# Optimization experiments

Measured on AMD Instinct MI355X. Metric: run time of the kernel, lower is better.

## Reference

```python
import jax, jax.numpy as jnp
import numpy as np

B, S, D = 2, 2048, 1024          # batch, seq, n_embd
E, GS, K = 8, 4, 2               # num_experts, group_size, top-k
H = 2 * D                        # hidden_dim of SharedExpertMLP
A = H // 16                      # adapt_dim = 128
G = E // GS                      # num_groups
LN_EPS = 1e-5


def _ln(z, g, b):
    mu = jnp.mean(z, -1, keepdims=True)
    v = jnp.mean((z - mu) ** 2, -1, keepdims=True)
    return (z - mu) * jax.lax.rsqrt(v + LN_EPS) * g + b


def setup_inputs() -> dict:
    key = jax.random.key(0)
    ks = jax.random.split(key, 12)
    s = float(D) ** -0.5
    sa = s * 0.01
    se = 0.01 * float(A) ** -0.5
    n = lambda k, shape, std: jax.random.normal(k, shape, jnp.float32) * std
    return {
        'x': jax.random.normal(ks[0], (B, S, D), jnp.float32),
        'W_up': n(ks[1], (H, D), s),
        'W_gate': n(ks[2], (H, D), s),
        'W_down': n(ks[3], (D, H), s),
        'W_pre': n(ks[4], (A, D), sa),
        'W_post': n(ks[5], (A, H), sa),
        'ln_g': jnp.ones((A,), jnp.float32),
        'ln_b': jnp.zeros((A,), jnp.float32),
        'W_aproj': n(ks[6], (H, A), sa),
        'A_exp': n(ks[7], (E, A, A), se),
        'ln_g_e': jnp.ones((E, A), jnp.float32),
        'ln_b_e': jnp.zeros((E, A), jnp.float32),
        'W_eproj': n(ks[8], (H, A), se),
        'W_oproj': n(ks[9], (D, H), se),
        'W_rg': n(ks[10], (G, D), 0.001),
        'W_re': n(ks[11], (GS, D), 0.001),
    }


def reference(x, W_up, W_gate, W_down, W_pre, W_post, ln_g, ln_b, W_aproj,
              A_exp, ln_g_e, ln_b_e, W_eproj, W_oproj, W_rg, W_re):
    silu = jax.nn.silu
    # ---- SharedExpertMLP ----
    up = x @ W_up.T
    gate = x @ W_gate.T
    hidden = silu(gate) * up                               # [B,S,H]
    adapt_in = _ln(x @ W_pre.T, ln_g, ln_b)                # [B,S,A]
    adapt_out = _ln(hidden @ W_post.T, ln_g, ln_b)         # [B,S,A]
    aw = silu(jnp.clip(jnp.einsum('bsa,bta->bst', adapt_in, adapt_out), -5.0, 5.0))
    adapt = jnp.einsum('bst,bta->bsa', aw, adapt_in)
    hidden = hidden + 0.1 * (adapt @ W_aproj.T)
    shared = hidden @ W_down.T                             # [B,S,D]
    # ---- HierarchicalRouter ----
    gl = x @ W_rg.T                                        # [B,S,G]
    gp = jax.nn.softmax(gl, -1)
    gw = jnp.max(gp, -1)                                   # top-1 group weight
    gidx = jnp.argmax(gp, -1)
    el = x @ W_re.T                                        # [B,S,GS]
    ep = jax.nn.softmax(el, -1)
    wloc, iloc = jax.lax.top_k(ep, K)
    eidx = gidx[..., None] * GS + iloc                     # [B,S,K] global expert ids
    wloc = wloc / (jnp.sum(wloc, -1, keepdims=True) + 1e-7)
    fw = gw[..., None] * wloc                              # final weights
    N = B * S
    dm = jnp.zeros((N, E), x.dtype).at[
        jnp.arange(N)[:, None], eidx.reshape(N, K)].set(fw.reshape(N, K))
    load = dm.sum(0)
    target = load.sum() / E
    router_loss = 0.001 * (jnp.mean((load - target) ** 2)
                           + jnp.mean(gl ** 2) + jnp.mean(el ** 2))
    dm = dm.reshape(B, S, E)
    # ---- ExpertGroup combine (vectorized masked gather/MLP/scatter) ----
    pre = x @ W_pre.T                                      # [B,S,A]
    h_e = jnp.einsum('bsa,eca->ebsc', pre, A_exp)          # per-expert adapter
    h_e = _ln(h_e, ln_g_e[:, None, None, :], ln_b_e[:, None, None, :])
    contrib = jnp.einsum('ebsc,hc->ebsh', h_e, W_eproj)    # [E,B,S,H]
    contrib = jnp.einsum('ebsh,dh->ebsd', contrib, W_oproj)
    w_e = jnp.moveaxis(dm, -1, 0)                          # [E,B,S]
    out = jnp.sum(dm, -1)[..., None] * shared + 0.1 * jnp.einsum('ebsd,ebs->bsd', contrib, w_e)
    return out, router_loss
```

## Files before the change

kernel.cpp:

```cpp
#include <hip/hip_runtime.h>
#include <hip/hip_bf16.h>
#include <math.h>

static constexpr int Bc = 2;
static constexpr int Sc = 2048;
static constexpr int Dc = 1024;
static constexpr int Hc = 2048;
static constexpr int Ac = 128;
static constexpr int Ec = 8;
static constexpr int GSc = 4;
static constexpr int Gc = 2;
static constexpr int Nc = Bc * Sc;
static constexpr float LN_EPSc = 1e-5f;
static constexpr int RBLK = 512;

typedef __attribute__((ext_vector_type(8))) short bf16x8;
typedef __attribute__((ext_vector_type(4))) float f32x4;
typedef __attribute__((ext_vector_type(4))) unsigned short us4;

__device__ __forceinline__ unsigned short f2b(float f) {
    union { float f; unsigned u; } v; v.f = f;
    return (unsigned short)((v.u + 0x7FFFu + ((v.u >> 16) & 1u)) >> 16);
}
__device__ __forceinline__ float b2f(unsigned short h) {
    union { unsigned u; float f; } v; v.u = (unsigned)h << 16; return v.f;
}
__device__ __forceinline__ float fsilu(float x) {
    return x / (1.f + __expf(-x));
}

#define GLOAD16(g, l) __builtin_amdgcn_global_load_lds( \
    (const __attribute__((address_space(1))) void*)(g), \
    (__attribute__((address_space(3))) void*)(l), 16, 0, 0)

template<int EPI>
__global__ __launch_bounds__(256, 4) void mgemm(
    const unsigned short* __restrict__ Ag, const unsigned short* __restrict__ Bg,
    void* __restrict__ Cg, int N, int K, int lda, int ldb, float alpha,
    float* __restrict__ aux, void* __restrict__ aux2,
    long long sA, long long sB, long long sC)
{
    __shared__ unsigned short As[128 * 32];
    __shared__ unsigned short Bs[128 * 32];
    const unsigned short* A = Ag + (long long)blockIdx.z * sA;
    const unsigned short* B = Bg + (long long)blockIdx.z * sB;
    float* fC = (float*)Cg + (long long)blockIdx.z * sC;
    unsigned short* usC = (unsigned short*)Cg + (long long)blockIdx.z * sC;

    const int nwg = gridDim.x * gridDim.y;
    const int flat = blockIdx.y * gridDim.x + blockIdx.x;
    const int swz = (flat & 7) * (nwg >> 3) + (flat >> 3);
    const int bx = swz % gridDim.x, by = swz / gridDim.x;
    const int bm = by * 128, bn = bx * 128;

    const int tid = threadIdx.x;
    const int w = tid >> 6, l = tid & 63;
    const int wm = (w >> 1) * 64, wn = (w & 1) * 64;
    const int fr = l & 15, g = l >> 4;

    const f32x4 zero = { 0.f, 0.f, 0.f, 0.f };
    f32x4 acc[4][4];
    #pragma unroll
    for (int i = 0; i < 4; ++i)
        #pragma unroll
        for (int j = 0; j < 4; ++j) acc[i][j] = zero;

    for (int k0 = 0; k0 < K; k0 += 32) {
        #pragma unroll
        for (int p = 0; p < 2; ++p) {
            const int c = p * 256 + tid;
            GLOAD16(A + (long long)(bm + (c >> 2)) * lda + k0 + (c & 3) * 8, &As[c * 8]);
            GLOAD16(B + (long long)(bn + (c >> 2)) * ldb + k0 + (c & 3) * 8, &Bs[c * 8]);
        }
        __syncthreads();
        bf16x8 af[4], bfv[4];
        #pragma unroll
        for (int i = 0; i < 4; ++i) {
            af[i]  = *(const bf16x8*)&As[(wm + i * 16 + fr) * 32 + g * 8];
            bfv[i] = *(const bf16x8*)&Bs[(wn + i * 16 + fr) * 32 + g * 8];
        }
        #pragma unroll
        for (int i = 0; i < 4; ++i)
            #pragma unroll
            for (int j = 0; j < 4; ++j)
                acc[i][j] = __builtin_amdgcn_mfma_f32_16x16x32_bf16(af[i], bfv[j], acc[i][j], 0, 0, 0);
        __syncthreads();
    }

    if (EPI == 9) {
        if (bn < 2 * Hc) {
            #pragma unroll
            for (int mi = 0; mi < 4; ++mi) {
                #pragma unroll
                for (int j = 0; j < 2; ++j) {
                    #pragma unroll
                    for (int jr = 0; jr < 4; ++jr) {
                        const long long row = bm + wm + mi * 16 + g * 4 + jr;
                        const long long colh = ((bn + wn) >> 1) + j * 16 + fr;
                        const float gv = acc[mi][2 * j][jr];
                        const float uv = acc[mi][2 * j + 1][jr];
                        usC[row * Hc + colh] = f2b(fsilu(gv) * uv);
                    }
                }
            }
        } else {
            unsigned short* preb = (unsigned short*)aux2;
            #pragma unroll
            for (int mi = 0; mi < 4; ++mi) {
                #pragma unroll
                for (int ni = 0; ni < 4; ++ni) {
                    #pragma unroll
                    for (int jr = 0; jr < 4; ++jr) {
                        const long long row = bm + wm + mi * 16 + g * 4 + jr;
                        const int lc = wn + ni * 16 + fr;
                        const float v = acc[mi][ni][jr];
                        aux[row * Ac + lc] = v;
                        preb[row * Ac + lc] = f2b(v);
                    }
                }
            }
        }
    } else {
        #pragma unroll
        for (int mi = 0; mi < 4; ++mi)
            #pragma unroll
            for (int ni = 0; ni < 4; ++ni)
                #pragma unroll
                for (int jr = 0; jr < 4; ++jr) {
                    const long long row = bm + wm + mi * 16 + g * 4 + jr;
                    const long long col = bn + wn + ni * 16 + fr;
                    const long long idx = row * (long long)N + col;
                    const float v = acc[mi][ni][jr];
                    if (EPI == 0) fC[idx] = v;
                    else usC[idx] = f2b(alpha * v);
                }
    }
}

__global__ __launch_bounds__(256, 2) void mgemm64(
    const unsigned short* __restrict__ Ag, const unsigned short* __restrict__ Bg,
    float* __restrict__ Cg, int N, int K, int lda, int ldb, int zmod,
    long long sA1, long long sB1, long long sC1,
    long long sA2, long long sB2, long long sC2)
{
    __shared__ unsigned short As[128 * 32];
    __shared__ unsigned short Bs[64 * 32];
    const int z1 = blockIdx.z % zmod, z2 = blockIdx.z / zmod;
    const unsigned short* A = Ag + (long long)z1 * sA1 + (long long)z2 * sA2;
    const unsigned short* B = Bg + (long long)z1 * sB1 + (long long)z2 * sB2;
    float* fC = Cg + (long long)z1 * sC1 + (long long)z2 * sC2;

    const int nwg = gridDim.x * gridDim.y;
    const int flat = blockIdx.y * gridDim.x + blockIdx.x;
    const int swz = (flat & 7) * (nwg >> 3) + (flat >> 3);
    const int bx = swz % gridDim.x, by = swz / gridDim.x;
    const int bm = by * 128, bn = bx * 64;

    const int tid = threadIdx.x;
    const int w = tid >> 6, l = tid & 63;
    const int wm = (w >> 1) * 64, wn = (w & 1) * 32;
    const int fr = l & 15, g = l >> 4;

    const f32x4 zero = { 0.f, 0.f, 0.f, 0.f };
    f32x4 acc[4][2];
    #pragma unroll
    for (int i = 0; i < 4; ++i)
        #pragma unroll
        for (int j = 0; j < 2; ++j) acc[i][j] = zero;

    for (int k0 = 0; k0 < K; k0 += 32) {
        #pragma unroll
        for (int p = 0; p < 2; ++p) {
            const int c = p * 256 + tid;
            GLOAD16(A + (long long)(bm + (c >> 2)) * lda + k0 + (c & 3) * 8, &As[c * 8]);
        }
        GLOAD16(B + (long long)(bn + (tid >> 2)) * ldb + k0 + (tid & 3) * 8, &Bs[tid * 8]);
        __syncthreads();
        bf16x8 af[4], bfv[2];
        #pragma unroll
        for (int i = 0; i < 4; ++i)
            af[i]  = *(const bf16x8*)&As[(wm + i * 16 + fr) * 32 + g * 8];
        #pragma unroll
        for (int j = 0; j < 2; ++j)
            bfv[j] = *(const bf16x8*)&Bs[(wn + j * 16 + fr) * 32 + g * 8];
        #pragma unroll
        for (int i = 0; i < 4; ++i)
            #pragma unroll
            for (int j = 0; j < 2; ++j)
                acc[i][j] = __builtin_amdgcn_mfma_f32_16x16x32_bf16(af[i], bfv[j], acc[i][j], 0, 0, 0);
        __syncthreads();
    }

    #pragma unroll
    for (int mi = 0; mi < 4; ++mi)
        #pragma unroll
        for (int ni = 0; ni < 2; ++ni)
            #pragma unroll
            for (int jr = 0; jr < 4; ++jr) {
                const long long row = bm + wm + mi * 16 + g * 4 + jr;
                const long long col = bn + wn + ni * 16 + fr;
                fC[row * (long long)N + col] = acc[mi][ni][jr];
            }
}

__global__ __launch_bounds__(256, 2) void fadapt_k(
    const unsigned short* __restrict__ adapt_in,
    const unsigned short* __restrict__ adapt_out,
    const unsigned short* __restrict__ adapt_inT,
    float* __restrict__ partial)
{
    __shared__ unsigned short P_lds[4 * 128 * 32];
    __shared__ unsigned short Bs[128 * 32];

    const int b = blockIdx.z;
    const int q0 = blockIdx.y * 128;
    const int t0 = blockIdx.x * 256;

    const unsigned short* Qg = adapt_in + (long long)b * Sc * Ac;
    const unsigned short* Kg = adapt_out + (long long)b * Sc * Ac;
    const unsigned short* Vt = adapt_inT + (long long)b * Ac * Sc;

    const int tid = threadIdx.x;
    const int w = tid >> 6, l = tid & 63;
    const int wm = (w >> 1) * 64, wn = (w & 1) * 64;
    const int fr = l & 15, g = l >> 4;

    bf16x8 qf[4][4];
    for (int ks = 0; ks < 4; ++ks) {
        #pragma unroll
        for (int p = 0; p < 2; ++p) {
            const int c = p * 256 + tid;
            GLOAD16(Qg + (long long)(q0 + (c >> 2)) * Ac + ks * 32 + (c & 3) * 8, &Bs[c * 8]);
        }
        __syncthreads();
        #pragma unroll
        for (int i = 0; i < 4; ++i)
            qf[i][ks] = *(const bf16x8*)&Bs[(wm + i * 16 + fr) * 32 + g * 8];
        __syncthreads();
    }

    const f32x4 zero = { 0.f, 0.f, 0.f, 0.f };
    f32x4 acc[4][4];
    #pragma unroll
    for (int i = 0; i < 4; ++i)
        #pragma unroll
        for (int j = 0; j < 4; ++j) acc[i][j] = zero;

    #pragma unroll 1
    for (int ts = 0; ts < 2; ++ts) {
        const int t1 = t0 + ts * 128;
        f32x4 sacc[4][4];
        #pragma unroll
        for (int i = 0; i < 4; ++i)
            #pragma unroll
            for (int j = 0; j < 4; ++j) sacc[i][j] = zero;
        for (int ks = 0; ks < 4; ++ks) {
            #pragma unroll
            for (int p = 0; p < 2; ++p) {
                const int c = p * 256 + tid;
                GLOAD16(Kg + (long long)(t1 + (c >> 2)) * Ac + ks * 32 + (c & 3) * 8, &Bs[c * 8]);
            }
            __syncthreads();
            bf16x8 bfv[4];
            #pragma unroll
            for (int j = 0; j < 4; ++j)
                bfv[j] = *(const bf16x8*)&Bs[(wn + j * 16 + fr) * 32 + g * 8];
            #pragma unroll
            for (int i = 0; i < 4; ++i)
                #pragma unroll
                for (int j = 0; j < 4; ++j)
                    sacc[i][j] = __builtin_amdgcn_mfma_f32_16x16x32_bf16(qf[i][ks], bfv[j], sacc[i][j], 0, 0, 0);
            __syncthreads();
        }
        #pragma unroll
        for (int mi = 0; mi < 4; ++mi) {
            #pragma unroll
            for (int ni = 0; ni < 4; ++ni) {
                const int t = wn + ni * 16 + fr;
                const int base = (t >> 5) * 4096 + (t & 31);
                #pragma unroll
                for (int jr = 0; jr < 4; ++jr) {
                    const int row = wm + mi * 16 + g * 4 + jr;
                    float v = sacc[mi][ni][jr];
                    v = fminf(fmaxf(v, -5.f), 5.f);
                    P_lds[base + row * 32] = f2b(fsilu(v));
                }
            }
        }
        __syncthreads();
        for (int ks = 0; ks < 4; ++ks) {
            #pragma unroll
            for (int p = 0; p < 2; ++p) {
                const int c = p * 256 + tid;
                GLOAD16(Vt + (long long)(c >> 2) * Sc + t1 + ks * 32 + (c & 3) * 8, &Bs[c * 8]);
            }
            __syncthreads();
            bf16x8 af[4], bfv[4];
            #pragma unroll
            for (int i = 0; i < 4; ++i)
                af[i] = *(const bf16x8*)&P_lds[ks * 4096 + (wm + i * 16 + fr) * 32 + g * 8];
            #pragma unroll
            for (int j = 0; j < 4; ++j)
                bfv[j] = *(const bf16x8*)&Bs[(wn + j * 16 + fr) * 32 + g * 8];
            #pragma unroll
            for (int i = 0; i < 4; ++i)
                #pragma unroll
                for (int j = 0; j < 4; ++j)
                    acc[i][j] = __builtin_amdgcn_mfma_f32_16x16x32_bf16(af[i], bfv[j], acc[i][j], 0, 0, 0);
            __syncthreads();
        }
    }

    float* op = partial + ((long long)blockIdx.x * Bc + b) * Sc * Ac;
    #pragma unroll
    for (int mi = 0; mi < 4; ++mi)
        #pragma unroll
        for (int ni = 0; ni < 4; ++ni)
            #pragma unroll
            for (int jr = 0; jr < 4; ++jr) {
                const long long row = q0 + wm + mi * 16 + g * 4 + jr;
                const long long col = wn + ni * 16 + fr;
                op[row * Ac + col] = acc[mi][ni][jr];
            }
}

__global__ __launch_bounds__(256, 2) void final_k(
    const unsigned short* __restrict__ hidden, const unsigned short* __restrict__ Wd,
    const unsigned short* __restrict__ adaptb, const unsigned short* __restrict__ Wdap,
    const unsigned short* __restrict__ h2v, const unsigned short* __restrict__ Wopep,
    const float* __restrict__ dmsum, float* __restrict__ out)
{
    __shared__ unsigned short As[128 * 32];
    __shared__ unsigned short Bs[64 * 32];

    const int nwg = gridDim.x * gridDim.y;
    const int flat = blockIdx.y * gridDim.x + blockIdx.x;
    const int swz = (flat & 7) * (nwg >> 3) + (flat >> 3);
    const int bx = swz % gridDim.x, by = swz / gridDim.x;
    const int bm = by * 128, bn = bx * 64;

    const int tid = threadIdx.x;
    const int w = tid >> 6, l = tid & 63;
    const int wm = (w >> 1) * 64, wn = (w & 1) * 32;
    const int fr = l & 15, g = l >> 4;

    const f32x4 zero = { 0.f, 0.f, 0.f, 0.f };
    f32x4 acc[4][2];
    #pragma unroll
    for (int i = 0; i < 4; ++i)
        #pragma unroll
        for (int j = 0; j < 2; ++j) acc[i][j] = zero;

    const unsigned short* Ap[3] = { hidden, adaptb, h2v };
    const unsigned short* Bp[3] = { Wd, Wdap, Wopep };
    const int Ks[3]  = { Hc, Ac, Ac };
    const int lds[3] = { Hc, Ac, Ac };

    #pragma unroll 1
    for (int ph = 0; ph < 3; ++ph) {
        if (ph == 2) {
            #pragma unroll
            for (int mi = 0; mi < 4; ++mi)
                #pragma unroll
                for (int jr = 0; jr < 4; ++jr) {
                    const float rs = dmsum[bm + wm + mi * 16 + g * 4 + jr];
                    #pragma unroll
                    for (int ni = 0; ni < 2; ++ni) acc[mi][ni][jr] *= rs;
                }
        }
        const unsigned short* A = Ap[ph];
        const unsigned short* B = Bp[ph];
        const int K = Ks[ph], ld = lds[ph];
        for (int k0 = 0; k0 < K; k0 += 32) {
            #pragma unroll
            for (int p = 0; p < 2; ++p) {
                const int c = p * 256 + tid;
                GLOAD16(A + (long long)(bm + (c >> 2)) * ld + k0 + (c & 3) * 8, &As[c * 8]);
            }
            GLOAD16(B + (long long)(bn + (tid >> 2)) * ld + k0 + (tid & 3) * 8, &Bs[tid * 8]);
            __syncthreads();
            bf16x8 af[4], bfv[2];
            #pragma unroll
            for (int i = 0; i < 4; ++i)
                af[i]  = *(const bf16x8*)&As[(wm + i * 16 + fr) * 32 + g * 8];
            #pragma unroll
            for (int j = 0; j < 2; ++j)
                bfv[j] = *(const bf16x8*)&Bs[(wn + j * 16 + fr) * 32 + g * 8];
            #pragma unroll
            for (int i = 0; i < 4; ++i)
                #pragma unroll
                for (int j = 0; j < 2; ++j)
                    acc[i][j] = __builtin_amdgcn_mfma_f32_16x16x32_bf16(af[i], bfv[j], acc[i][j], 0, 0, 0);
            __syncthreads();
        }
    }

    #pragma unroll
    for (int mi = 0; mi < 4; ++mi)
        #pragma unroll
        for (int ni = 0; ni < 2; ++ni)
            #pragma unroll
            for (int jr = 0; jr < 4; ++jr) {
                const long long row = bm + wm + mi * 16 + g * 4 + jr;
                const long long col = bn + wn + ni * 16 + fr;
                out[row * (long long)Dc + col] = acc[mi][ni][jr];
            }
}

template<int NP, int BF>
__global__ __launch_bounds__(256) void reduce_k(const float* __restrict__ in,
                                                void* __restrict__ outp,
                                                long long pstride, int n4, float alpha)
{
    for (int i = blockIdx.x * 256 + threadIdx.x; i < n4; i += gridDim.x * 256) {
        float4 s = ((const float4*)in)[i];
        #pragma unroll
        for (int p = 1; p < NP; ++p) {
            const float4 v = ((const float4*)(in + (long long)p * pstride))[i];
            s.x += v.x; s.y += v.y; s.z += v.z; s.w += v.w;
        }
        s.x *= alpha; s.y *= alpha; s.z *= alpha; s.w *= alpha;
        if (BF) {
            us4 o = { f2b(s.x), f2b(s.y), f2b(s.z), f2b(s.w) };
            ((us4*)outp)[i] = o;
        } else {
            ((float4*)outp)[i] = s;
        }
    }
}

struct CastJobs {
    const float* src[4];
    unsigned short* dst[4];
    int n4[4];
};
__global__ __launch_bounds__(256) void cast_k(CastJobs jobs) {
    const int b = blockIdx.y;
    const float4* s = (const float4*)jobs.src[b];
    us4* d = (us4*)jobs.dst[b];
    const int n = jobs.n4[b];
    for (int i = blockIdx.x * 256 + threadIdx.x; i < n; i += gridDim.x * 256) {
        const float4 v = s[i];
        us4 o;
        o.x = f2b(v.x); o.y = f2b(v.y); o.z = f2b(v.z); o.w = f2b(v.w);
        d[i] = o;
    }
}

__global__ __launch_bounds__(256) void gucast_k(const float* __restrict__ Wg,
                                                const float* __restrict__ Wu,
                                                const float* __restrict__ Wpre,
                                                unsigned short* __restrict__ Wcat)
{
    const int r = blockIdx.x;
    const float* src;
    int srcrow;
    if (r < 2 * Hc) {
        const int b = r >> 5, w = r & 31;
        src = (w < 16) ? Wg : Wu;
        srcrow = b * 16 + (w & 15);
    } else {
        src = Wpre;
        srcrow = r - 2 * Hc;
    }
    const float4 v = ((const float4*)(src + (long long)srcrow * Dc))[threadIdx.x];
    us4 o;
    o.x = f2b(v.x); o.y = f2b(v.y); o.z = f2b(v.z); o.w = f2b(v.w);
    ((us4*)(Wcat + (long long)r * Dc))[threadIdx.x] = o;
}

__global__ __launch_bounds__(256) void ct_k(const float* __restrict__ in0,
                                            const float* __restrict__ in1,
                                            unsigned short* __restrict__ out0,
                                            unsigned short* __restrict__ out1)
{
    const float* in = blockIdx.z ? in1 : in0;
    unsigned short* out = blockIdx.z ? out1 : out0;
    const int t0 = blockIdx.x * 64, a0 = blockIdx.y * 64;
    __shared__ float T[64][68];
    const int rr = threadIdx.x >> 4, cc = (threadIdx.x & 15) * 4;
    #pragma unroll
    for (int p = 0; p < 4; ++p) {
        const int row = p * 16 + rr;
        *(float4*)&T[row][cc] = *(const float4*)&in[(long long)(t0 + row) * Ac + a0 + cc];
    }
    __syncthreads();
    #pragma unroll
    for (int p = 0; p < 4; ++p) {
        const int ar = p * 16 + rr;
        us4 o;
        o.x = f2b(T[cc + 0][ar]); o.y = f2b(T[cc + 1][ar]);
        o.z = f2b(T[cc + 2][ar]); o.w = f2b(T[cc + 3][ar]);
        *(us4*)&out[(long long)(a0 + ar) * Hc + t0 + cc] = o;
    }
}

__global__ __launch_bounds__(64) void ln_k(const float* __restrict__ in, unsigned short* __restrict__ out,
                                           const float* __restrict__ gg, const float* __restrict__ bb)
{
    const int row = blockIdx.x;
    const int lane = threadIdx.x;
    const float z0 = in[(long long)row * 128 + lane];
    const float z1 = in[(long long)row * 128 + 64 + lane];
    float s = z0 + z1;
    for (int o = 32; o > 0; o >>= 1) s += __shfl_down(s, o, 64);
    s = __shfl(s, 0, 64);
    const float mu = s * (1.f / 128.f);
    const float d0 = z0 - mu, d1 = z1 - mu;
    float v = d0 * d0 + d1 * d1;
    for (int o = 32; o > 0; o >>= 1) v += __shfl_down(v, o, 64);
    v = __shfl(v, 0, 64);
    const float r = rsqrtf(v * (1.f / 128.f) + LN_EPSc);
    out[(long long)row * 128 + lane] = f2b(d0 * r * gg[lane] + bb[lane]);
    out[(long long)row * 128 + 64 + lane] = f2b(d1 * r * gg[lane + 64] + bb[lane + 64]);
}

__global__ __launch_bounds__(64) void redln_k(const float* __restrict__ in,
                                              unsigned short* __restrict__ out,
                                              const float* __restrict__ gg,
                                              const float* __restrict__ bb,
                                              long long pstride)
{
    const int row = blockIdx.x;
    const int lane = threadIdx.x;
    float z0 = 0.f, z1 = 0.f;
    #pragma unroll
    for (int p = 0; p < 4; ++p) {
        z0 += in[p * pstride + (long long)row * 128 + lane];
        z1 += in[p * pstride + (long long)row * 128 + 64 + lane];
    }
    float s = z0 + z1;
    for (int o = 32; o > 0; o >>= 1) s += __shfl_down(s, o, 64);
    s = __shfl(s, 0, 64);
    const float mu = s * (1.f / 128.f);
    const float d0 = z0 - mu, d1 = z1 - mu;
    float v = d0 * d0 + d1 * d1;
    for (int o = 32; o > 0; o >>= 1) v += __shfl_down(v, o, 64);
    v = __shfl(v, 0, 64);
    const float r = rsqrtf(v * (1.f / 128.f) + LN_EPSc);
    out[(long long)row * 128 + lane] = f2b(d0 * r * gg[lane] + bb[lane]);
    out[(long long)row * 128 + 64 + lane] = f2b(d1 * r * gg[lane + 64] + bb[lane + 64]);
}

__global__ __launch_bounds__(256) void trans_k(const unsigned short* __restrict__ in,
                                               unsigned short* __restrict__ out)
{
    const int z = blockIdx.z;
    const int t0 = blockIdx.x * 64, a0 = blockIdx.y * 64;
    __shared__ unsigned short T[64][72];
    const unsigned short* ip = in + (long long)z * Sc * Ac;
    unsigned short* op = out + (long long)z * Ac * Sc;
    const int rr = threadIdx.x >> 4, cc = (threadIdx.x & 15) * 4;
    #pragma unroll
    for (int p = 0; p < 4; ++p) {
        const int row = p * 16 + rr;
        *(us4*)&T[row][cc] = *(const us4*)&ip[(long long)(t0 + row) * Ac + a0 + cc];
    }
    __syncthreads();
    #pragma unroll
    for (int p = 0; p < 4; ++p) {
        const int arow = p * 16 + rr;
        us4 o;
        o.x = T[cc + 0][arow]; o.y = T[cc + 1][arow];
        o.z = T[cc + 2][arow]; o.w = T[cc + 3][arow];
        *(us4*)&op[(long long)(a0 + arow) * Sc + t0 + cc] = o;
    }
}

__global__ __launch_bounds__(256) void router_k(const float* __restrict__ x,
                                                const float* __restrict__ W_rg,
                                                const float* __restrict__ W_re,
                                                int* __restrict__ eidx, float* __restrict__ fw,
                                                float* __restrict__ dmsum,
                                                float* __restrict__ rpart,
                                                unsigned short* __restrict__ xb)
{
    const int wv = threadIdx.x >> 6;
    const int lane = threadIdx.x & 63;
    float load8[8] = {0.f, 0.f, 0.f, 0.f, 0.f, 0.f, 0.f, 0.f};
    float sqg = 0.f, sqe = 0.f;

    #pragma unroll
    for (int it = 0; it < 2; ++it) {
        const int t = blockIdx.x * 8 + wv * 2 + it;
        const float* xr = x + (long long)t * Dc;
        float a0 = 0, a1 = 0, a2 = 0, a3 = 0, a4 = 0, a5 = 0;
        #pragma unroll
        for (int j = 0; j < 16; ++j) {
            const int d = lane + 64 * j;
            const float xv = xr[d];
            xb[(long long)t * Dc + d] = f2b(xv);
            a0 += xv * W_rg[d];          a1 += xv * W_rg[Dc + d];
            a2 += xv * W_re[d];          a3 += xv * W_re[Dc + d];
            a4 += xv * W_re[2 * Dc + d]; a5 += xv * W_re[3 * Dc + d];
        }
        #pragma unroll
        for (int o = 32; o > 0; o >>= 1) {
            a0 += __shfl_xor(a0, o, 64); a1 += __shfl_xor(a1, o, 64);
            a2 += __shfl_xor(a2, o, 64); a3 += __shfl_xor(a3, o, 64);
            a4 += __shfl_xor(a4, o, 64); a5 += __shfl_xor(a5, o, 64);
        }
        if (lane == 0) {
            const float gl0 = a0, gl1 = a1;
            const float m = fmaxf(gl0, gl1);
            const float e0 = expf(gl0 - m), e1 = expf(gl1 - m);
            const float inv = 1.f / (e0 + e1);
            const float gp0 = e0 * inv, gp1 = e1 * inv;
            const int gidx = (gl1 > gl0) ? 1 : 0;
            const float gw = fmaxf(gp0, gp1);
            float el[4] = { a2, a3, a4, a5 };
            const float me = fmaxf(fmaxf(el[0], el[1]), fmaxf(el[2], el[3]));
            float ep[4]; float se = 0.f;
            #pragma unroll
            for (int i = 0; i < 4; ++i) { ep[i] = expf(el[i] - me); se += ep[i]; }
            const float invs = 1.f / se;
            #pragma unroll
            for (int i = 0; i < 4; ++i) ep[i] *= invs;
            int i0 = 0;
            #pragma unroll
            for (int i = 1; i < 4; ++i) if (ep[i] > ep[i0]) i0 = i;
            int i1 = -1;
            #pragma unroll
            for (int i = 0; i < 4; ++i) { if (i == i0) continue; if (i1 < 0 || ep[i] > ep[i1]) i1 = i; }
            const float w0 = ep[i0], w1 = ep[i1];
            const float sn = w0 + w1 + 1e-7f;
            const float f0 = gw * w0 / sn, f1 = gw * w1 / sn;
            const int ei0 = gidx * GSc + i0, ei1 = gidx * GSc + i1;
            eidx[t * 2] = ei0; eidx[t * 2 + 1] = ei1;
            fw[t * 2] = f0; fw[t * 2 + 1] = f1;
            dmsum[t] = f0 + f1;
            #pragma unroll
            for (int e = 0; e < 8; ++e)
                load8[e] += ((e == ei0) ? f0 : 0.f) + ((e == ei1) ? f1 : 0.f);
            sqg += gl0 * gl0 + gl1 * gl1;
            sqe += el[0] * el[0] + el[1] * el[1] + el[2] * el[2] + el[3] * el[3];
        }
    }
    __shared__ float sh[4][10];
    if (lane == 0) {
        #pragma unroll
        for (int e = 0; e < 8; ++e) sh[wv][e] = load8[e];
        sh[wv][8] = sqg; sh[wv][9] = sqe;
    }
    __syncthreads();
    if (threadIdx.x < 10) {
        rpart[blockIdx.x * 10 + threadIdx.x] =
            sh[0][threadIdx.x] + sh[1][threadIdx.x] + sh[2][threadIdx.x] + sh[3][threadIdx.x];
    }
}

__global__ __launch_bounds__(512) void loss_k(const float* __restrict__ rpart,
                                              float* __restrict__ out_loss)
{
    const int tid = threadIdx.x;
    const int lane = tid & 63, wv = tid >> 6;
    float v[10];
    #pragma unroll
    for (int c = 0; c < 10; ++c) v[c] = rpart[tid * 10 + c];
    #pragma unroll
    for (int o = 32; o > 0; o >>= 1)
        #pragma unroll
        for (int c = 0; c < 10; ++c) v[c] += __shfl_xor(v[c], o, 64);
    __shared__ float sh[8][10];
    if (lane == 0) {
        #pragma unroll
        for (int c = 0; c < 10; ++c) sh[wv][c] = v[c];
    }
    __syncthreads();
    if (tid == 0) {
        float load[8]; float sqg = 0.f, sqe = 0.f;
        #pragma unroll
        for (int e = 0; e < 8; ++e) load[e] = 0.f;
        for (int wvi = 0; wvi < 8; ++wvi) {
            #pragma unroll
            for (int e = 0; e < 8; ++e) load[e] += sh[wvi][e];
            sqg += sh[wvi][8]; sqe += sh[wvi][9];
        }
        float s = 0.f;
        for (int e = 0; e < Ec; ++e) s += load[e];
        const float tgt = s / (float)Ec;
        float var = 0.f;
        for (int e = 0; e < Ec; ++e) { const float d = load[e] - tgt; var += d * d; }
        var /= (float)Ec;
        const float l = var + sqg / (float)(Nc * Gc) + sqe / (float)(Nc * GSc);
        *out_loss = 0.001f * l;
    }
}

__global__ __launch_bounds__(128) void combine_k(const float* __restrict__ h_dense,
                                                 const float* __restrict__ ln_g_e,
                                                 const float* __restrict__ ln_b_e,
                                                 const int* __restrict__ eidx,
                                                 const float* __restrict__ fw,
                                                 unsigned short* __restrict__ h2)
{
    const int t = blockIdx.x;
    const int tid = threadIdx.x;
    __shared__ float red[2];

    float acc = 0.f;
    #pragma unroll
    for (int slot = 0; slot < 2; ++slot) {
        const int e = eidx[t * 2 + slot];
        const float w = fw[t * 2 + slot];
        const float h = h_dense[((long long)e * Nc + t) * 128 + tid];
        float v = h;
        for (int o = 32; o > 0; o >>= 1) v += __shfl_down(v, o, 64);
        if ((tid & 63) == 0) red[tid >> 6] = v;
        __syncthreads();
        const float mu = (red[0] + red[1]) * (1.f / 128.f);
        __syncthreads();
        const float d = h - mu;
        v = d * d;
        for (int o = 32; o > 0; o >>= 1) v += __shfl_down(v, o, 64);
        if ((tid & 63) == 0) red[tid >> 6] = v;
        __syncthreads();
        const float var = (red[0] + red[1]) * (1.f / 128.f);
        __syncthreads();
        acc += w * (d * rsqrtf(var + LN_EPSc) * ln_g_e[e * 128 + tid] + ln_b_e[e * 128 + tid]);
    }
    h2[(long long)t * 128 + tid] = f2b(acc);
}

extern "C" void kernel_launch(void* const* d_in, const int* in_sizes, int n_in,
                              void* d_out, int out_size, void* d_ws, size_t ws_size,
                              hipStream_t stream)
{
    const float* x       = (const float*)d_in[0];
    const float* W_up    = (const float*)d_in[1];
    const float* W_gate  = (const float*)d_in[2];
    const float* W_down  = (const float*)d_in[3];
    const float* W_pre   = (const float*)d_in[4];
    const float* W_post  = (const float*)d_in[5];
    const float* ln_g    = (const float*)d_in[6];
    const float* ln_b    = (const float*)d_in[7];
    const float* W_aproj = (const float*)d_in[8];
    const float* A_exp   = (const float*)d_in[9];
    const float* ln_g_e  = (const float*)d_in[10];
    const float* ln_b_e  = (const float*)d_in[11];
    const float* W_eproj = (const float*)d_in[12];
    const float* W_oproj = (const float*)d_in[13];
    const float* W_rg    = (const float*)d_in[14];
    const float* W_re    = (const float*)d_in[15];

    float* out = (float*)d_out;

    char* p = (char*)d_ws;
    auto alloc = [&](size_t bytes) { void* r = (void*)p; p += (bytes + 255) & ~(size_t)255; return r; };
    float* pre      = (float*)alloc((size_t)Nc * Ac * 4);
    float* h_dense  = (float*)alloc((size_t)Ec * Nc * Ac * 4);
    float* rpart    = (float*)alloc((size_t)RBLK * 10 * 4);
    float* fw       = (float*)alloc((size_t)Nc * 2 * 4);
    float* dmsum    = (float*)alloc((size_t)Nc * 4);
    int*   eidx     = (int*)alloc((size_t)Nc * 2 * 4);
    unsigned short* xb      = (unsigned short*)alloc((size_t)Nc * Dc * 2);
    unsigned short* Wcat_b  = (unsigned short*)alloc((size_t)(2 * Hc + Ac) * Dc * 2);
    unsigned short* Wd_b    = (unsigned short*)alloc((size_t)Dc * Hc * 2);
    unsigned short* Wop_b   = (unsigned short*)alloc((size_t)Dc * Hc * 2);
    unsigned short* Wpost_b = (unsigned short*)alloc((size_t)Ac * Hc * 2);
    unsigned short* WapT_b  = (unsigned short*)alloc((size_t)Ac * Hc * 2);
    unsigned short* WepT_b  = (unsigned short*)alloc((size_t)Ac * Hc * 2);
    unsigned short* Wdap_b  = (unsigned short*)alloc((size_t)Dc * Ac * 2);
    unsigned short* Wopep_b = (unsigned short*)alloc((size_t)Dc * Ac * 2);
    unsigned short* Aexp_b  = (unsigned short*)alloc((size_t)Ec * Ac * Ac * 2);
    unsigned short* pre_b   = (unsigned short*)alloc((size_t)Nc * Ac * 2);
    unsigned short* hidden  = (unsigned short*)alloc((size_t)Nc * Hc * 2);
    unsigned short* adapt_in  = (unsigned short*)alloc((size_t)Nc * Ac * 2);
    unsigned short* adapt_inT = (unsigned short*)alloc((size_t)Nc * Ac * 2);
    unsigned short* adapt_out = (unsigned short*)alloc((size_t)Nc * Ac * 2);
    unsigned short* adaptb    = (unsigned short*)alloc((size_t)Nc * Ac * 2);
    unsigned short* h2        = (unsigned short*)alloc((size_t)Nc * Ac * 2);

    float* wprepP = h_dense;
    float* postP  = h_dense;
    float* adaptP = h_dense;

    CastJobs jobs;
    jobs.src[0] = W_down;  jobs.dst[0] = Wd_b;    jobs.n4[0] = Dc * Hc / 4;
    jobs.src[1] = W_oproj; jobs.dst[1] = Wop_b;   jobs.n4[1] = Dc * Hc / 4;
    jobs.src[2] = W_post;  jobs.dst[2] = Wpost_b; jobs.n4[2] = Ac * Hc / 4;
    jobs.src[3] = A_exp;   jobs.dst[3] = Aexp_b;  jobs.n4[3] = Ec * Ac * Ac / 4;
    cast_k<<<dim3(128, 4), 256, 0, stream>>>(jobs);
    gucast_k<<<2 * Hc + Ac, 256, 0, stream>>>(W_gate, W_up, W_pre, Wcat_b);
    ct_k<<<dim3(Hc / 64, Ac / 64, 2), 256, 0, stream>>>(W_aproj, W_eproj, WapT_b, WepT_b);

    router_k<<<RBLK, 256, 0, stream>>>(x, W_rg, W_re, eidx, fw, dmsum, rpart, xb);
    loss_k<<<1, 512, 0, stream>>>(rpart, out + (size_t)Nc * Dc);

    mgemm64<<<dim3(2, 8, 8), 256, 0, stream>>>(Wd_b, WapT_b, wprepP, Ac, 512, Hc, Hc,
        2,
        (long long)Dc * Hc, (long long)Ac * Hc, (long long)Dc * Ac,
        512, 512, (long long)2 * Dc * Ac);
    reduce_k<4, 1><<<256, 256, 0, stream>>>(wprepP, Wdap_b,
        (long long)2 * Dc * Ac, 2 * Dc * Ac / 4, 0.1f);

    mgemm<9><<<dim3(33, 32), 256, 0, stream>>>(xb, Wcat_b, hidden, 2 * Hc + Ac, Dc, Dc, Dc, 0.f,
        pre, pre_b, 0, 0, 0);
    ln_k<<<Nc, 64, 0, stream>>>(pre, adapt_in, ln_g, ln_b);
    trans_k<<<dim3(Sc / 64, Ac / 64, Bc), 256, 0, stream>>>(adapt_in, adapt_inT);

    mgemm64<<<dim3(2, 32, 4), 256, 0, stream>>>(hidden, Wpost_b, postP, Ac, 512, Hc, Hc,
        8, 512, 512, (long long)Nc * Ac, 0, 0, 0);
    redln_k<<<Nc, 64, 0, stream>>>(postP, adapt_out, ln_g, ln_b, (long long)Nc * Ac);

    mgemm64<<<dim3(2, 32, Ec), 256, 0, stream>>>(pre_b, Aexp_b, h_dense, Ac, Ac, Ac, Ac,
        16, 0, (long long)Ac * Ac, (long long)Nc * Ac, 0, 0, 0);
    combine_k<<<Nc, 128, 0, stream>>>(h_dense, ln_g_e, ln_b_e, eidx, fw, h2);

    fadapt_k<<<dim3(8, 16, 2), 256, 0, stream>>>(adapt_in, adapt_out, adapt_inT, adaptP);
    reduce_k<8, 1><<<512, 256, 0, stream>>>(adaptP, adaptb,
        (long long)2 * Sc * Ac, 2 * Sc * Ac / 4, 1.f);

    final_k<<<dim3(Dc / 64, Nc / 128), 256, 0, stream>>>(
        hidden, Wd_b, adaptb, Wdap_b, h2, Wopep_b, dmsum, out);
}
```

Measured before the change: 200.7 us.

## Double GEMM K-tile with XOR-swizzled LDS, merge prep kernels, fuse LN with transpose

The main GEMM and the final GEMM now stage 64-wide K tiles instead of 32, halving the number of barrier pairs per K sweep, and use an XOR swizzle on the LDS chunk index to cut bank conflicts. The three weight cast/transpose kernels are merged into one launch. LayerNorm of the pre-adapter output is fused with its transpose into one kernel, and the warp reductions switch to xor-shuffles. Doubling LDS per block may lower occupancy on the mgemm kernel, which declares four blocks per CU.

```diff
diff --git a/kernel.cpp b/kernel.cpp
--- a/kernel.cpp
+++ b/kernel.cpp
@@ -40,8 +40,8 @@
     float* __restrict__ aux, void* __restrict__ aux2,
     long long sA, long long sB, long long sC)
 {
-    __shared__ unsigned short As[128 * 32];
-    __shared__ unsigned short Bs[128 * 32];
+    __shared__ unsigned short As[128 * 64];
+    __shared__ unsigned short Bs[128 * 64];
     const unsigned short* A = Ag + (long long)blockIdx.z * sA;
     const unsigned short* B = Bg + (long long)blockIdx.z * sB;
     float* fC = (float*)Cg + (long long)blockIdx.z * sC;
@@ -65,25 +65,32 @@
         #pragma unroll
         for (int j = 0; j < 4; ++j) acc[i][j] = zero;
 
-    for (int k0 = 0; k0 < K; k0 += 32) {
-        #pragma unroll
-        for (int p = 0; p < 2; ++p) {
+    for (int k0 = 0; k0 < K; k0 += 64) {
+        #pragma unroll
+        for (int p = 0; p < 4; ++p) {
             const int c = p * 256 + tid;
-            GLOAD16(A + (long long)(bm + (c >> 2)) * lda + k0 + (c & 3) * 8, &As[c * 8]);
-            GLOAD16(B + (long long)(bn + (c >> 2)) * ldb + k0 + (c & 3) * 8, &Bs[c * 8]);
-        }
-        __syncthreads();
-        bf16x8 af[4], bfv[4];
-        #pragma unroll
-        for (int i = 0; i < 4; ++i) {
-            af[i]  = *(const bf16x8*)&As[(wm + i * 16 + fr) * 32 + g * 8];
-            bfv[i] = *(const bf16x8*)&Bs[(wn + i * 16 + fr) * 32 + g * 8];
-        }
-        #pragma unroll
-        for (int i = 0; i < 4; ++i)
-            #pragma unroll
-            for (int j = 0; j < 4; ++j)
-                acc[i][j] = __builtin_amdgcn_mfma_f32_16x16x32_bf16(af[i], bfv[j], acc[i][j], 0, 0, 0);
+            const int row = c >> 3;
+            const int gch = (c & 7) ^ ((c >> 4) & 7);
+            GLOAD16(A + (long long)(bm + row) * lda + k0 + gch * 8, &As[c * 8]);
+            GLOAD16(B + (long long)(bn + row) * ldb + k0 + gch * 8, &Bs[c * 8]);
+        }
+        __syncthreads();
+        #pragma unroll
+        for (int h = 0; h < 2; ++h) {
+            bf16x8 af[4], bfv[4];
+            #pragma unroll
+            for (int i = 0; i < 4; ++i) {
+                const int ra = wm + i * 16 + fr;
+                af[i]  = *(const bf16x8*)&As[ra * 64 + ((h * 4 + g) ^ ((ra >> 1) & 7)) * 8];
+                const int rb = wn + i * 16 + fr;
+                bfv[i] = *(const bf16x8*)&Bs[rb * 64 + ((h * 4 + g) ^ ((rb >> 1) & 7)) * 8];
+            }
+            #pragma unroll
+            for (int i = 0; i < 4; ++i)
+                #pragma unroll
+                for (int j = 0; j < 4; ++j)
+                    acc[i][j] = __builtin_amdgcn_mfma_f32_16x16x32_bf16(af[i], bfv[j], acc[i][j], 0, 0, 0);
+        }
         __syncthreads();
     }
 
@@ -330,8 +337,8 @@
     const unsigned short* __restrict__ h2v, const unsigned short* __restrict__ Wopep,
     const float* __restrict__ dmsum, float* __restrict__ out)
 {
-    __shared__ unsigned short As[128 * 32];
-    __shared__ unsigned short Bs[64 * 32];
+    __shared__ unsigned short As[128 * 64];
+    __shared__ unsigned short Bs[64 * 64];
 
     const int nwg = gridDim.x * gridDim.y;
     const int flat = blockIdx.y * gridDim.x + blockIdx.x;
@@ -371,26 +378,41 @@
         const unsigned short* A = Ap[ph];
         const unsigned short* B = Bp[ph];
         const int K = Ks[ph], ld = lds[ph];
-        for (int k0 = 0; k0 < K; k0 += 32) {
+        for (int k0 = 0; k0 < K; k0 += 64) {
+            #pragma unroll
+            for (int p = 0; p < 4; ++p) {
+                const int c = p * 256 + tid;
+                const int row = c >> 3;
+                const int gch = (c & 7) ^ ((c >> 4) & 7);
+                GLOAD16(A + (long long)(bm + row) * ld + k0 + gch * 8, &As[c * 8]);
+            }
             #pragma unroll
             for (int p = 0; p < 2; ++p) {
                 const int c = p * 256 + tid;
-                GLOAD16(A + (long long)(bm + (c >> 2)) * ld + k0 + (c & 3) * 8, &As[c * 8]);
-            }
-            GLOAD16(B + (long long)(bn + (tid >> 2)) * ld + k0 + (tid & 3) * 8, &Bs[tid * 8]);
+                const int row = c >> 3;
+                const int gch = (c & 7) ^ ((c >> 4) & 7);
+                GLOAD16(B + (long long)(bn + row) * ld + k0 + gch * 8, &Bs[c * 8]);
+            }
             __syncthreads();
-            bf16x8 af[4], bfv[2];
-            #pragma unroll
-            for (int i = 0; i < 4; ++i)
-                af[i]  = *(const bf16x8*)&As[(wm + i * 16 + fr) * 32 + g * 8];
-            #pragma unroll
-            for (int j = 0; j < 2; ++j)
-                bfv[j] = *(const bf16x8*)&Bs[(wn + j * 16 + fr) * 32 + g * 8];
-            #pragma unroll
-            for (int i = 0; i < 4; ++i)
-                #pragma unroll
-                for (int j = 0; j < 2; ++j)
-                    acc[i][j] = __builtin_amdgcn_mfma_f32_16x16x32_bf16(af[i], bfv[j], acc[i][j], 0, 0, 0);
+            #pragma unroll
+            for (int h = 0; h < 2; ++h) {
+                bf16x8 af[4], bfv[2];
+                #pragma unroll
+                for (int i = 0; i < 4; ++i) {
+                    const int ra = wm + i * 16 + fr;
+                    af[i]  = *(const bf16x8*)&As[ra * 64 + ((h * 4 + g) ^ ((ra >> 1) & 7)) * 8];
+                }
+                #pragma unroll
+                for (int j = 0; j < 2; ++j) {
+                    const int rb = wn + j * 16 + fr;
+                    bfv[j] = *(const bf16x8*)&Bs[rb * 64 + ((h * 4 + g) ^ ((rb >> 1) & 7)) * 8];
+                }
+                #pragma unroll
+                for (int i = 0; i < 4; ++i)
+                    #pragma unroll
+                    for (int j = 0; j < 2; ++j)
+                        acc[i][j] = __builtin_amdgcn_mfma_f32_16x16x32_bf16(af[i], bfv[j], acc[i][j], 0, 0, 0);
+            }
             __syncthreads();
         }
     }
@@ -429,90 +451,117 @@
     }
 }
 
-struct CastJobs {
-    const float* src[4];
-    unsigned short* dst[4];
-    int n4[4];
+struct PrepArgs {
+    const float* csrc[4]; unsigned short* cdst[4]; int cn4[4];
+    const float* Wg; const float* Wu; const float* Wpre; unsigned short* Wcat;
+    const float* tin0; const float* tin1; unsigned short* tout0; unsigned short* tout1;
 };
-__global__ __launch_bounds__(256) void cast_k(CastJobs jobs) {
-    const int b = blockIdx.y;
-    const float4* s = (const float4*)jobs.src[b];
-    us4* d = (us4*)jobs.dst[b];
-    const int n = jobs.n4[b];
-    for (int i = blockIdx.x * 256 + threadIdx.x; i < n; i += gridDim.x * 256) {
-        const float4 v = s[i];
-        us4 o;
-        o.x = f2b(v.x); o.y = f2b(v.y); o.z = f2b(v.z); o.w = f2b(v.w);
-        d[i] = o;
-    }
-}
-
-__global__ __launch_bounds__(256) void gucast_k(const float* __restrict__ Wg,
-                                                const float* __restrict__ Wu,
-                                                const float* __restrict__ Wpre,
-                                                unsigned short* __restrict__ Wcat)
-{
-    const int r = blockIdx.x;
-    const float* src;
-    int srcrow;
-    if (r < 2 * Hc) {
-        const int b = r >> 5, w = r & 31;
-        src = (w < 16) ? Wg : Wu;
-        srcrow = b * 16 + (w & 15);
+__global__ __launch_bounds__(256) void prep_k(PrepArgs a)
+{
+    __shared__ float T[64][68];
+    const int y = blockIdx.y;
+    if (y < 4) {
+        const float4* s = (const float4*)a.csrc[y];
+        us4* d = (us4*)a.cdst[y];
+        const int n = a.cn4[y];
+        for (int i = blockIdx.x * 256 + threadIdx.x; i < n; i += gridDim.x * 256) {
+            const float4 v = s[i];
+            us4 o;
+            o.x = f2b(v.x); o.y = f2b(v.y); o.z = f2b(v.z); o.w = f2b(v.w);
+            d[i] = o;
+        }
+    } else if (y == 4) {
+        const int total = (2 * Hc + Ac) * 256;
+        for (int u = blockIdx.x * 256 + threadIdx.x; u < total; u += gridDim.x * 256) {
+            const int r = u >> 8, t = u & 255;
+            const float* src; int srcrow;
+            if (r < 2 * Hc) {
+                const int b = r >> 5, wq = r & 31;
+                src = (wq < 16) ? a.Wg : a.Wu;
+                srcrow = b * 16 + (wq & 15);
+            } else {
+                src = a.Wpre;
+                srcrow = r - 2 * Hc;
+            }
+            const float4 v = ((const float4*)(src + (long long)srcrow * Dc))[t];
+            us4 o;
+            o.x = f2b(v.x); o.y = f2b(v.y); o.z = f2b(v.z); o.w = f2b(v.w);
+            ((us4*)(a.Wcat + (long long)r * Dc))[t] = o;
+        }
     } else {
-        src = Wpre;
-        srcrow = r - 2 * Hc;
-    }
-    const float4 v = ((const float4*)(src + (long long)srcrow * Dc))[threadIdx.x];
-    us4 o;
-    o.x = f2b(v.x); o.y = f2b(v.y); o.z = f2b(v.z); o.w = f2b(v.w);
-    ((us4*)(Wcat + (long long)r * Dc))[threadIdx.x] = o;
-}
-
-__global__ __launch_bounds__(256) void ct_k(const float* __restrict__ in0,
-                                            const float* __restrict__ in1,
-                                            unsigned short* __restrict__ out0,
-                                            unsigned short* __restrict__ out1)
-{
-    const float* in = blockIdx.z ? in1 : in0;
-    unsigned short* out = blockIdx.z ? out1 : out0;
-    const int t0 = blockIdx.x * 64, a0 = blockIdx.y * 64;
-    __shared__ float T[64][68];
-    const int rr = threadIdx.x >> 4, cc = (threadIdx.x & 15) * 4;
-    #pragma unroll
-    for (int p = 0; p < 4; ++p) {
-        const int row = p * 16 + rr;
-        *(float4*)&T[row][cc] = *(const float4*)&in[(long long)(t0 + row) * Ac + a0 + cc];
+        const int rr = threadIdx.x >> 4, cc = (threadIdx.x & 15) * 4;
+        for (int tb = blockIdx.x; tb < 128; tb += gridDim.x) {
+            const int z = tb >> 6, rem = tb & 63;
+            const int a0 = (rem >> 5) * 64, t0 = (rem & 31) * 64;
+            const float* in = z ? a.tin1 : a.tin0;
+            unsigned short* outp = z ? a.tout1 : a.tout0;
+            __syncthreads();
+            #pragma unroll
+            for (int p = 0; p < 4; ++p) {
+                const int row = p * 16 + rr;
+                *(float4*)&T[row][cc] = *(const float4*)&in[(long long)(t0 + row) * Ac + a0 + cc];
+            }
+            __syncthreads();
+            #pragma unroll
+            for (int p = 0; p < 4; ++p) {
+                const int ar = p * 16 + rr;
+                us4 o;
+                o.x = f2b(T[cc + 0][ar]); o.y = f2b(T[cc + 1][ar]);
+                o.z = f2b(T[cc + 2][ar]); o.w = f2b(T[cc + 3][ar]);
+                *(us4*)&outp[(long long)(a0 + ar) * Hc + t0 + cc] = o;
+            }
+        }
+    }
+}
+
+__global__ __launch_bounds__(256) void lntr_k(const float* __restrict__ in,
+                                              unsigned short* __restrict__ outn,
+                                              unsigned short* __restrict__ outt,
+                                              const float* __restrict__ gg,
+                                              const float* __restrict__ bb)
+{
+    __shared__ unsigned short L[64][130];
+    const int z = blockIdx.y;
+    const int t0 = blockIdx.x * 64;
+    const int wv = threadIdx.x >> 6, lane = threadIdx.x & 63;
+    const float g0 = gg[lane], g1 = gg[lane + 64];
+    const float b0 = bb[lane], b1 = bb[lane + 64];
+
+    #pragma unroll 4
+    for (int it = 0; it < 16; ++it) {
+        const int row = wv * 16 + it;
+        const long long gr = (long long)(z * Sc + t0 + row) * 128;
+        const float z0 = in[gr + lane], z1 = in[gr + 64 + lane];
+        float s = z0 + z1;
+        #pragma unroll
+        for (int o = 32; o > 0; o >>= 1) s += __shfl_xor(s, o, 64);
+        const float mu = s * (1.f / 128.f);
+        const float d0 = z0 - mu, d1 = z1 - mu;
+        float v = d0 * d0 + d1 * d1;
+        #pragma unroll
+        for (int o = 32; o > 0; o >>= 1) v += __shfl_xor(v, o, 64);
+        const float r = rsqrtf(v * (1.f / 128.f) + LN_EPSc);
+        L[row][lane] = f2b(d0 * r * g0 + b0);
+        L[row][lane + 64] = f2b(d1 * r * g1 + b1);
     }
     __syncthreads();
-    #pragma unroll
-    for (int p = 0; p < 4; ++p) {
-        const int ar = p * 16 + rr;
-        us4 o;
-        o.x = f2b(T[cc + 0][ar]); o.y = f2b(T[cc + 1][ar]);
-        o.z = f2b(T[cc + 2][ar]); o.w = f2b(T[cc + 3][ar]);
-        *(us4*)&out[(long long)(a0 + ar) * Hc + t0 + cc] = o;
-    }
-}
-
-__global__ __launch_bounds__(64) void ln_k(const float* __restrict__ in, unsigned short* __restrict__ out,
-                                           const float* __restrict__ gg, const float* __restrict__ bb)
-{
-    const int row = blockIdx.x;
-    const int lane = threadIdx.x;
-    const float z0 = in[(long long)row * 128 + lane];
-    const float z1 = in[(long long)row * 128 + 64 + lane];
-    float s = z0 + z1;
-    for (int o = 32; o > 0; o >>= 1) s += __shfl_down(s, o, 64);
-    s = __shfl(s, 0, 64);
-    const float mu = s * (1.f / 128.f);
-    const float d0 = z0 - mu, d1 = z1 - mu;
-    float v = d0 * d0 + d1 * d1;
-    for (int o = 32; o > 0; o >>= 1) v += __shfl_down(v, o, 64);
-    v = __shfl(v, 0, 64);
-    const float r = rsqrtf(v * (1.f / 128.f) + LN_EPSc);
-    out[(long long)row * 128 + lane] = f2b(d0 * r * gg[lane] + bb[lane]);
-    out[(long long)row * 128 + 64 + lane] = f2b(d1 * r * gg[lane + 64] + bb[lane + 64]);
+    {
+        const int row = threadIdx.x >> 2, seg = (threadIdx.x & 3) * 32;
+        #pragma unroll
+        for (int j = 0; j < 8; ++j)
+            *(us4*)&outn[(long long)(z * Sc + t0 + row) * 128 + seg + j * 4] =
+                *(const us4*)&L[row][seg + j * 4];
+    }
+    {
+        const int a = threadIdx.x >> 1, tt0 = (threadIdx.x & 1) * 32;
+        #pragma unroll
+        for (int j4 = 0; j4 < 8; ++j4) {
+            us4 o;
+            o.x = L[tt0 + j4 * 4 + 0][a]; o.y = L[tt0 + j4 * 4 + 1][a];
+            o.z = L[tt0 + j4 * 4 + 2][a]; o.w = L[tt0 + j4 * 4 + 3][a];
+            *(us4*)&outt[(long long)z * Ac * Sc + (long long)a * Sc + t0 + tt0 + j4 * 4] = o;
+        }
+    }
 }
 
 __global__ __launch_bounds__(64) void redln_k(const float* __restrict__ in,
@@ -530,41 +579,14 @@
         z1 += in[p * pstride + (long long)row * 128 + 64 + lane];
     }
     float s = z0 + z1;
-    for (int o = 32; o > 0; o >>= 1) s += __shfl_down(s, o, 64);
-    s = __shfl(s, 0, 64);
+    for (int o = 32; o > 0; o >>= 1) s += __shfl_xor(s, o, 64);
     const float mu = s * (1.f / 128.f);
     const float d0 = z0 - mu, d1 = z1 - mu;
     float v = d0 * d0 + d1 * d1;
-    for (int o = 32; o > 0; o >>= 1) v += __shfl_down(v, o, 64);
-    v = __shfl(v, 0, 64);
+    for (int o = 32; o > 0; o >>= 1) v += __shfl_xor(v, o, 64);
     const float r = rsqrtf(v * (1.f / 128.f) + LN_EPSc);
     out[(long long)row * 128 + lane] = f2b(d0 * r * gg[lane] + bb[lane]);
     out[(long long)row * 128 + 64 + lane] = f2b(d1 * r * gg[lane + 64] + bb[lane + 64]);
-}
-
-__global__ __launch_bounds__(256) void trans_k(const unsigned short* __restrict__ in,
-                                               unsigned short* __restrict__ out)
-{
-    const int z = blockIdx.z;
-    const int t0 = blockIdx.x * 64, a0 = blockIdx.y * 64;
-    __shared__ unsigned short T[64][72];
-    const unsigned short* ip = in + (long long)z * Sc * Ac;
-    unsigned short* op = out + (long long)z * Ac * Sc;
-    const int rr = threadIdx.x >> 4, cc = (threadIdx.x & 15) * 4;
-    #pragma unroll
-    for (int p = 0; p < 4; ++p) {
-        const int row = p * 16 + rr;
-        *(us4*)&T[row][cc] = *(const us4*)&ip[(long long)(t0 + row) * Ac + a0 + cc];
-    }
-    __syncthreads();
-    #pragma unroll
-    for (int p = 0; p < 4; ++p) {
-        const int arow = p * 16 + rr;
-        us4 o;
-        o.x = T[cc + 0][arow]; o.y = T[cc + 1][arow];
-        o.z = T[cc + 2][arow]; o.w = T[cc + 3][arow];
-        *(us4*)&op[(long long)(a0 + arow) * Sc + t0 + cc] = o;
-    }
 }
 
 __global__ __launch_bounds__(256) void router_k(const float* __restrict__ x,
@@ -775,14 +797,14 @@
     float* postP  = h_dense;
     float* adaptP = h_dense;
 
-    CastJobs jobs;
-    jobs.src[0] = W_down;  jobs.dst[0] = Wd_b;    jobs.n4[0] = Dc * Hc / 4;
-    jobs.src[1] = W_oproj; jobs.dst[1] = Wop_b;   jobs.n4[1] = Dc * Hc / 4;
-    jobs.src[2] = W_post;  jobs.dst[2] = Wpost_b; jobs.n4[2] = Ac * Hc / 4;
-    jobs.src[3] = A_exp;   jobs.dst[3] = Aexp_b;  jobs.n4[3] = Ec * Ac * Ac / 4;
-    cast_k<<<dim3(128, 4), 256, 0, stream>>>(jobs);
-    gucast_k<<<2 * Hc + Ac, 256, 0, stream>>>(W_gate, W_up, W_pre, Wcat_b);
-    ct_k<<<dim3(Hc / 64, Ac / 64, 2), 256, 0, stream>>>(W_aproj, W_eproj, WapT_b, WepT_b);
+    PrepArgs pa;
+    pa.csrc[0] = W_down;  pa.cdst[0] = Wd_b;    pa.cn4[0] = Dc * Hc / 4;
+    pa.csrc[1] = W_oproj; pa.cdst[1] = Wop_b;   pa.cn4[1] = Dc * Hc / 4;
+    pa.csrc[2] = W_post;  pa.cdst[2] = Wpost_b; pa.cn4[2] = Ac * Hc / 4;
+    pa.csrc[3] = A_exp;   pa.cdst[3] = Aexp_b;  pa.cn4[3] = Ec * Ac * Ac / 4;
+    pa.Wg = W_gate; pa.Wu = W_up; pa.Wpre = W_pre; pa.Wcat = Wcat_b;
+    pa.tin0 = W_aproj; pa.tin1 = W_eproj; pa.tout0 = WapT_b; pa.tout1 = WepT_b;
+    prep_k<<<dim3(64, 6), 256, 0, stream>>>(pa);
 
     router_k<<<RBLK, 256, 0, stream>>>(x, W_rg, W_re, eidx, fw, dmsum, rpart, xb);
     loss_k<<<1, 512, 0, stream>>>(rpart, out + (size_t)Nc * Dc);
@@ -796,8 +818,7 @@
 
     mgemm<9><<<dim3(33, 32), 256, 0, stream>>>(xb, Wcat_b, hidden, 2 * Hc + Ac, Dc, Dc, Dc, 0.f,
         pre, pre_b, 0, 0, 0);
-    ln_k<<<Nc, 64, 0, stream>>>(pre, adapt_in, ln_g, ln_b);
-    trans_k<<<dim3(Sc / 64, Ac / 64, Bc), 256, 0, stream>>>(adapt_in, adapt_inT);
+    lntr_k<<<dim3(Sc / 64, Bc), 256, 0, stream>>>(pre, adapt_in, adapt_inT, ln_g, ln_b);
 
     mgemm64<<<dim3(2, 32, 4), 256, 0, stream>>>(hidden, Wpost_b, postP, Ac, 512, Hc, Hc,
         8, 512, 512, (long long)Nc * Ac, 0, 0, 0);
```

After: 198.1 us. Within noise of the previous version (-1.3%).
